# Performance work log

Measured on AMD Instinct MI355X. Metric: run time of the kernel, lower is better.

The kernel has to match this reference:

```python
import jax, jax.numpy as jnp
import numpy as np

INV_TEMPERATURE = 0.125  # 1/sqrt(head_dim=64)


def setup_inputs() -> dict:
    key = jax.random.key(0)
    kq, kk, kv, kp, km = jax.random.split(key, 5)
    B, H, S, D = 8, 8, 2048, 64
    q = jax.random.normal(kq, (B, H, S, D), dtype=jnp.float32)
    k = jax.random.normal(kk, (B, H, S, D), dtype=jnp.float32)
    v = jax.random.normal(kv, (B, H, S, D), dtype=jnp.float32)
    pos_scores = jax.random.normal(kp, (1, H, S, S), dtype=jnp.float32)
    mask = jax.random.uniform(km, (1, 1, S, S), dtype=jnp.float32)
    return {"q": q, "k": k, "v": v, "pos_scores": pos_scores, "mask": mask}


def reference(q, k, v, pos_scores, mask):
    # sim = (q k^T) * inv_temp + pos_scores, then multiplicative mask
    sim = jnp.einsum('bhid,bhjd->bhij', q, k) * INV_TEMPERATURE
    sim = mask * (sim + pos_scores)
    attn = jax.nn.softmax(sim, axis=-1)
    out = jnp.einsum('bhij,bhjd->bhid', attn, v)
    return out
```

## Files before the change

kernel.cpp:

```cpp
#include <hip/hip_runtime.h>

constexpr int SEQ = 2048;
constexpr int HD  = 64;
constexpr int NH  = 8;
constexpr int NB  = 8;
constexpr int BM  = 64;
constexpr int BN  = 64;
constexpr int KST = 72;
constexpr float INV_T = 0.125f;
constexpr float LOG2E = 1.4426950408889634f;

typedef __attribute__((ext_vector_type(8))) short bf16x8;
typedef __attribute__((ext_vector_type(8))) short s16x8;
typedef __attribute__((ext_vector_type(4))) short s16x4;
typedef __attribute__((ext_vector_type(4))) float f32x4;

__device__ __forceinline__ short f2bf(float f) {
  unsigned u = __builtin_bit_cast(unsigned, f);
  u += 0x7fffu + ((u >> 16) & 1u);
  return (short)(u >> 16);
}
__device__ __forceinline__ float bf2f(short s) {
  unsigned u = ((unsigned)(unsigned short)s) << 16;
  return __builtin_bit_cast(float, u);
}
__device__ __forceinline__ float fast_exp2(float x) {
#if __has_builtin(__builtin_amdgcn_exp2f)
  return __builtin_amdgcn_exp2f(x);
#else
  return exp2f(x);
#endif
}

__global__ __launch_bounds__(256)
void prep_kv(const float* __restrict__ k, const float* __restrict__ v,
             unsigned short* __restrict__ kb, unsigned short* __restrict__ vt)
{
  __shared__ unsigned short t[HD * KST];
  const int bh = blockIdx.y, jt = blockIdx.x, tid = threadIdx.x;
  const size_t base = (size_t)bh * SEQ * HD + (size_t)jt * BN * HD;

  {
    const float* kp = k + base + 16 * tid;
    unsigned short ko[16];
    for (int e = 0; e < 4; ++e) {
      f32x4 x = *(const f32x4*)(kp + 4 * e);
      for (int c = 0; c < 4; ++c) ko[4 * e + c] = (unsigned short)f2bf(x[c]);
    }
    *(s16x8*)(kb + base + 16 * tid)     = *(const s16x8*)&ko[0];
    *(s16x8*)(kb + base + 16 * tid + 8) = *(const s16x8*)&ko[8];
  }
  {
    const float* vp = v + base + 16 * tid;
    const int j = tid >> 2, d0 = (tid & 3) * 16;
    for (int e = 0; e < 4; ++e) {
      f32x4 x = *(const f32x4*)(vp + 4 * e);
      for (int c = 0; c < 4; ++c) t[(d0 + 4 * e + c) * KST + j] = (unsigned short)f2bf(x[c]);
    }
  }
  __syncthreads();
  {
    const int d = tid >> 2, ch = tid & 3;
    const size_t ob = (size_t)bh * HD * SEQ + (size_t)d * SEQ + jt * BN + ch * 16;
    *(s16x8*)(vt + ob)     = *(const s16x8*)&t[d * KST + ch * 16];
    *(s16x8*)(vt + ob + 8) = *(const s16x8*)&t[d * KST + ch * 16 + 8];
  }
}

__global__ __launch_bounds__(256, 4)
void attn_main(const float* __restrict__ q, const unsigned short* __restrict__ kb,
               const unsigned short* __restrict__ vt,
               const float* __restrict__ pos, const float* __restrict__ mask,
               float* __restrict__ out)
{
  __shared__ unsigned short lds_k[BN * KST];
  __shared__ unsigned short lds_v[HD * KST];

  const int n = blockIdx.x;
  const int x = n & 7, b = (n >> 3) & 7, G = n >> 6;
  const int g = G * 8 + x;
  const int h = g >> 5, it = g & 31;
  const int bh = b * NH + h;
  const int i0 = it * BM;

  const int tid = threadIdx.x, wave = tid >> 6, lane = tid & 63;
  const int quad = lane >> 4, lq = lane & 15;

  bf16x8 aq[2];
  {
    const float* qp = q + ((size_t)bh * SEQ + i0 + wave * 16 + lq) * HD + quad * 8;
    for (int k0 = 0; k0 < 2; ++k0) {
      f32x4 xv = *(const f32x4*)(qp + k0 * 32);
      f32x4 yv = *(const f32x4*)(qp + k0 * 32 + 4);
      for (int c = 0; c < 4; ++c) {
        aq[k0][c]     = f2bf(xv[c] * INV_T);
        aq[k0][4 + c] = f2bf(yv[c] * INV_T);
      }
    }
  }

  f32x4 oacc[4];
  for (int d = 0; d < 4; ++d) oacc[d] = (f32x4){0.f, 0.f, 0.f, 0.f};
  float lrun = 0.f;

  const int lw = (tid >> 3) * KST + (tid & 7) * 8;
  const unsigned short* kgb = kb + (size_t)bh * SEQ * HD + 8 * tid;
  const unsigned short* vgb = vt + (size_t)bh * HD * SEQ + (tid >> 3) * SEQ + (tid & 7) * 8;

  const int irow = i0 + wave * 16 + lq;
  const float* mrow = mask + (size_t)irow * SEQ + quad * 4;
  const float* prow = pos + ((size_t)h * SEQ + irow) * SEQ + quad * 4;

  unsigned short* lds_p = lds_k;
  const int pbase = wave * (16 * KST);

  s16x8 kx0, kx1, vx0, vx1;
  f32x4 m4[4], p4[4];

  kx0 = *(const s16x8*)(kgb);
  kx1 = *(const s16x8*)(kgb + 2048);
  vx0 = *(const s16x8*)(vgb);
  vx1 = *(const s16x8*)(vgb + 32 * SEQ);
#pragma unroll
  for (int s = 0; s < 4; ++s) {
    m4[s] = *(const f32x4*)(mrow + s * 16);
    p4[s] = *(const f32x4*)(prow + s * 16);
  }

  for (int jt = 0; jt < SEQ / BN; ++jt) {
    const int jn = (jt + 1) & 31;
    __syncthreads();
    *(s16x8*)&lds_k[lw]            = kx0;
    *(s16x8*)&lds_k[lw + 32 * KST] = kx1;
    *(s16x8*)&lds_v[lw]            = vx0;
    *(s16x8*)&lds_v[lw + 32 * KST] = vx1;
    __syncthreads();

    kx0 = *(const s16x8*)(kgb + jn * 4096);
    kx1 = *(const s16x8*)(kgb + jn * 4096 + 2048);
    vx0 = *(const s16x8*)(vgb + jn * 64);
    vx1 = *(const s16x8*)(vgb + jn * 64 + 32 * SEQ);

    f32x4 sa[4];
#pragma unroll
    for (int s = 0; s < 4; ++s) sa[s] = (f32x4){0.f, 0.f, 0.f, 0.f};
#pragma unroll
    for (int k0 = 0; k0 < 2; ++k0)
#pragma unroll
      for (int s = 0; s < 4; ++s) {
        bf16x8 bk = *(const bf16x8*)&lds_k[(s * 16 + lq) * KST + k0 * 32 + quad * 8];
        sa[s] = __builtin_amdgcn_mfma_f32_16x16x32_bf16(bk, aq[k0], sa[s], 0, 0, 0);
      }
    __syncthreads();

    const float* mjn = mrow + jn * 64;
    const float* pjn = prow + jn * 64;
#pragma unroll
    for (int s = 0; s < 4; ++s) {
      f32x4 mm = m4[s];
      f32x4 pp = p4[s];
      m4[s] = *(const f32x4*)(mjn + s * 16);
      p4[s] = *(const f32x4*)(pjn + s * 16);
      s16x4 pb;
      float ps = 0.f;
#pragma unroll
      for (int r = 0; r < 4; ++r) {
        float t = mm[r] * LOG2E;
        float a = fmaf(t, sa[s][r], t * pp[r]);
        float p = fast_exp2(a);
        unsigned pu = __builtin_bit_cast(unsigned, p);
        pb[r] = (short)(pu >> 16);
        ps += __builtin_bit_cast(float, pu & 0xffff0000u);
      }
      lrun += ps;
      *(s16x4*)&lds_p[pbase + lq * KST + s * 16 + quad * 4] = pb;
    }
    asm volatile("s_waitcnt lgkmcnt(0)" ::: "memory");

#pragma unroll
    for (int k0 = 0; k0 < 2; ++k0) {
      bf16x8 ap = *(const bf16x8*)&lds_p[pbase + lq * KST + k0 * 32 + quad * 8];
#pragma unroll
      for (int d = 0; d < 4; ++d) {
        bf16x8 bv = *(const bf16x8*)&lds_v[(d * 16 + lq) * KST + k0 * 32 + quad * 8];
        oacc[d] = __builtin_amdgcn_mfma_f32_16x16x32_bf16(ap, bv, oacc[d], 0, 0, 0);
      }
    }
  }

  lrun += __shfl_xor(lrun, 16);
  lrun += __shfl_xor(lrun, 32);

#pragma unroll
  for (int r = 0; r < 4; ++r) {
    const float lv = __shfl(lrun, quad * 4 + r);
    const float inv = 1.0f / lv;
    float* orow = out + ((size_t)bh * SEQ + i0 + wave * 16 + quad * 4 + r) * HD + lq;
#pragma unroll
    for (int d = 0; d < 4; ++d) orow[d * 16] = oacc[d][r] * inv;
  }
}

__global__ __launch_bounds__(256, 2)
void attn_fused(const float* __restrict__ q, const float* __restrict__ kk,
                const float* __restrict__ vv, const float* __restrict__ pos,
                const float* __restrict__ mask, float* __restrict__ out)
{
  __shared__ short lds_k[BN * KST];
  __shared__ short lds_v[HD * KST];
  __shared__ short lds_p[4][16 * KST];
  const int bh = blockIdx.y, h = bh & (NH - 1);
  const int i0 = blockIdx.x * BM;
  const int tid = threadIdx.x, wave = tid >> 6, lane = tid & 63;
  const int quad = lane >> 4, lq = lane & 15;
  bf16x8 aq[2];
  {
    const float* qp = q + ((size_t)bh * SEQ + i0 + wave * 16 + lq) * HD + quad * 8;
    for (int k0 = 0; k0 < 2; ++k0) {
      f32x4 xv = *(const f32x4*)(qp + k0 * 32);
      f32x4 yv = *(const f32x4*)(qp + k0 * 32 + 4);
      for (int j = 0; j < 4; ++j) { aq[k0][j] = f2bf(xv[j] * INV_T); aq[k0][4 + j] = f2bf(yv[j] * INV_T); }
    }
  }
  f32x4 oacc[4];
  for (int d = 0; d < 4; ++d) oacc[d] = (f32x4){0.f, 0.f, 0.f, 0.f};
  float mrun[4] = {-INFINITY, -INFINITY, -INFINITY, -INFINITY};
  float lrun[4] = {0.f, 0.f, 0.f, 0.f};
  const size_t kvbase = (size_t)bh * SEQ * HD;
  for (int jt = 0; jt < SEQ / BN; ++jt) {
    const int j0 = jt * BN;
    __syncthreads();
    for (int e = 0; e < 4; ++e) {
      int idx = e * 256 + tid, j = idx >> 4, d4 = (idx & 15) << 2;
      f32x4 kf = *(const f32x4*)(kk + kvbase + (size_t)(j0 + j) * HD + d4);
      s16x4 ks;
      for (int c = 0; c < 4; ++c) ks[c] = f2bf(kf[c]);
      *(s16x4*)&lds_k[j * KST + d4] = ks;
      f32x4 vf = *(const f32x4*)(vv + kvbase + (size_t)(j0 + j) * HD + d4);
      for (int c = 0; c < 4; ++c) lds_v[(d4 + c) * KST + j] = f2bf(vf[c]);
    }
    __syncthreads();
    float mk[4][4], pz[4][4];
    for (int r = 0; r < 4; ++r) {
      const int i = i0 + wave * 16 + quad * 4 + r;
      const float* mrow = mask + (size_t)i * SEQ + j0 + lq;
      const float* prow = pos + ((size_t)h * SEQ + i) * SEQ + j0 + lq;
      for (int s = 0; s < 4; ++s) { mk[r][s] = mrow[s * 16]; pz[r][s] = prow[s * 16]; }
    }
    f32x4 sa[4];
    for (int s = 0; s < 4; ++s) sa[s] = (f32x4){0.f, 0.f, 0.f, 0.f};
    for (int k0 = 0; k0 < 2; ++k0)
      for (int s = 0; s < 4; ++s) {
        bf16x8 bk = *(const bf16x8*)&lds_k[(s * 16 + lq) * KST + k0 * 32 + quad * 8];
        sa[s] = __builtin_amdgcn_mfma_f32_16x16x32_bf16(aq[k0], bk, sa[s], 0, 0, 0);
      }
    for (int r = 0; r < 4; ++r) {
      float s0 = mk[r][0] * (sa[0][r] + pz[r][0]);
      float s1 = mk[r][1] * (sa[1][r] + pz[r][1]);
      float s2 = mk[r][2] * (sa[2][r] + pz[r][2]);
      float s3 = mk[r][3] * (sa[3][r] + pz[r][3]);
      float rm = fmaxf(fmaxf(s0, s1), fmaxf(s2, s3));
      for (int off = 1; off < 16; off <<= 1) rm = fmaxf(rm, __shfl_xor(rm, off));
      float mn = fmaxf(mrun[r], rm);
      float al = __expf(mrun[r] - mn);
      mrun[r] = mn;
      short p0 = f2bf(__expf(s0 - mn)), p1 = f2bf(__expf(s1 - mn));
      short p2 = f2bf(__expf(s2 - mn)), p3 = f2bf(__expf(s3 - mn));
      float ps = bf2f(p0) + bf2f(p1) + bf2f(p2) + bf2f(p3);
      for (int off = 1; off < 16; off <<= 1) ps += __shfl_xor(ps, off);
      lrun[r] = lrun[r] * al + ps;
      for (int d = 0; d < 4; ++d) oacc[d][r] *= al;
      short* pr = &lds_p[wave][(quad * 4 + r) * KST + lq];
      pr[0] = p0; pr[16] = p1; pr[32] = p2; pr[48] = p3;
    }
    asm volatile("s_waitcnt lgkmcnt(0)" ::: "memory");
    for (int k0 = 0; k0 < 2; ++k0) {
      bf16x8 ap = *(const bf16x8*)&lds_p[wave][lq * KST + k0 * 32 + quad * 8];
      for (int d = 0; d < 4; ++d) {
        bf16x8 bv = *(const bf16x8*)&lds_v[(d * 16 + lq) * KST + k0 * 32 + quad * 8];
        oacc[d] = __builtin_amdgcn_mfma_f32_16x16x32_bf16(ap, bv, oacc[d], 0, 0, 0);
      }
    }
  }
  for (int r = 0; r < 4; ++r) {
    const int i = i0 + wave * 16 + quad * 4 + r;
    const float inv = 1.0f / lrun[r];
    float* orow = out + ((size_t)bh * SEQ + i) * HD + lq;
    for (int d = 0; d < 4; ++d) orow[d * 16] = oacc[d][r] * inv;
  }
}

extern "C" void kernel_launch(void* const* d_in, const int* in_sizes, int n_in,
                              void* d_out, int out_size, void* d_ws, size_t ws_size,
                              hipStream_t stream) {
  const float* q    = (const float*)d_in[0];
  const float* k    = (const float*)d_in[1];
  const float* v    = (const float*)d_in[2];
  const float* pos  = (const float*)d_in[3];
  const float* mask = (const float*)d_in[4];
  float* out = (float*)d_out;

  const size_t kv_elems = (size_t)NB * NH * SEQ * HD;
  const size_t kb_bytes = kv_elems * 2;
  const size_t need = 2 * kb_bytes;

  if (ws_size >= need) {
    unsigned short* kb = (unsigned short*)d_ws;
    unsigned short* vt = (unsigned short*)((char*)d_ws + kb_bytes);
    prep_kv<<<dim3(SEQ / BN, NB * NH), dim3(256), 0, stream>>>(k, v, kb, vt);
    attn_main<<<dim3(NB * NH * SEQ / BM), dim3(256), 0, stream>>>(q, kb, vt, pos, mask, out);
  } else {
    attn_fused<<<dim3(SEQ / BM, NB * NH), dim3(256), 0, stream>>>(q, k, v, pos, mask, out);
  }
}
```

Baseline: 515.7 us.

## Double-buffer K/V tiles in LDS and give P its own buffer

Allocates two LDS buffers for the K and V tiles plus a separate buffer for P. The next tile is stored into the alternate buffer while the current one is consumed, which cuts the per-iteration barriers from three to one and lets global prefetch run two tiles ahead. In exchange LDS use per block rises, which may lower occupancy below the four blocks per CU set in launch bounds, and more registers stay live.

```diff
diff --git a/kernel.cpp b/kernel.cpp
--- a/kernel.cpp
+++ b/kernel.cpp
@@ -73,8 +73,9 @@
                const float* __restrict__ pos, const float* __restrict__ mask,
                float* __restrict__ out)
 {
-  __shared__ unsigned short lds_k[BN * KST];
-  __shared__ unsigned short lds_v[HD * KST];
+  __shared__ unsigned short lds_k[2][BN * KST];
+  __shared__ unsigned short lds_v[2][HD * KST];
+  __shared__ unsigned short lds_p[4 * 16 * KST];
 
   const int n = blockIdx.x;
   const int x = n & 7, b = (n >> 3) & 7, G = n >> 6;
@@ -111,7 +112,6 @@
   const float* mrow = mask + (size_t)irow * SEQ + quad * 4;
   const float* prow = pos + ((size_t)h * SEQ + irow) * SEQ + quad * 4;
 
-  unsigned short* lds_p = lds_k;
   const int pbase = wave * (16 * KST);
 
   s16x8 kx0, kx1, vx0, vx1;
@@ -126,33 +126,41 @@
     m4[s] = *(const f32x4*)(mrow + s * 16);
     p4[s] = *(const f32x4*)(prow + s * 16);
   }
+  *(s16x8*)&lds_k[0][lw]            = kx0;
+  *(s16x8*)&lds_k[0][lw + 32 * KST] = kx1;
+  *(s16x8*)&lds_v[0][lw]            = vx0;
+  *(s16x8*)&lds_v[0][lw + 32 * KST] = vx1;
+  kx0 = *(const s16x8*)(kgb + 4096);
+  kx1 = *(const s16x8*)(kgb + 4096 + 2048);
+  vx0 = *(const s16x8*)(vgb + 64);
+  vx1 = *(const s16x8*)(vgb + 64 + 32 * SEQ);
+  __syncthreads();
 
   for (int jt = 0; jt < SEQ / BN; ++jt) {
+    const int cur = jt & 1, nxt = cur ^ 1;
+    const int j2 = (jt + 2) & 31;
+
+    f32x4 sa[4];
+#pragma unroll
+    for (int s = 0; s < 4; ++s) sa[s] = (f32x4){0.f, 0.f, 0.f, 0.f};
+#pragma unroll
+    for (int k0 = 0; k0 < 2; ++k0)
+#pragma unroll
+      for (int s = 0; s < 4; ++s) {
+        bf16x8 bk = *(const bf16x8*)&lds_k[cur][(s * 16 + lq) * KST + k0 * 32 + quad * 8];
+        sa[s] = __builtin_amdgcn_mfma_f32_16x16x32_bf16(bk, aq[k0], sa[s], 0, 0, 0);
+      }
+
+    *(s16x8*)&lds_k[nxt][lw]            = kx0;
+    *(s16x8*)&lds_k[nxt][lw + 32 * KST] = kx1;
+    *(s16x8*)&lds_v[nxt][lw]            = vx0;
+    *(s16x8*)&lds_v[nxt][lw + 32 * KST] = vx1;
+    kx0 = *(const s16x8*)(kgb + j2 * 4096);
+    kx1 = *(const s16x8*)(kgb + j2 * 4096 + 2048);
+    vx0 = *(const s16x8*)(vgb + j2 * 64);
+    vx1 = *(const s16x8*)(vgb + j2 * 64 + 32 * SEQ);
+
     const int jn = (jt + 1) & 31;
-    __syncthreads();
-    *(s16x8*)&lds_k[lw]            = kx0;
-    *(s16x8*)&lds_k[lw + 32 * KST] = kx1;
-    *(s16x8*)&lds_v[lw]            = vx0;
-    *(s16x8*)&lds_v[lw + 32 * KST] = vx1;
-    __syncthreads();
-
-    kx0 = *(const s16x8*)(kgb + jn * 4096);
-    kx1 = *(const s16x8*)(kgb + jn * 4096 + 2048);
-    vx0 = *(const s16x8*)(vgb + jn * 64);
-    vx1 = *(const s16x8*)(vgb + jn * 64 + 32 * SEQ);
-
-    f32x4 sa[4];
-#pragma unroll
-    for (int s = 0; s < 4; ++s) sa[s] = (f32x4){0.f, 0.f, 0.f, 0.f};
-#pragma unroll
-    for (int k0 = 0; k0 < 2; ++k0)
-#pragma unroll
-      for (int s = 0; s < 4; ++s) {
-        bf16x8 bk = *(const bf16x8*)&lds_k[(s * 16 + lq) * KST + k0 * 32 + quad * 8];
-        sa[s] = __builtin_amdgcn_mfma_f32_16x16x32_bf16(bk, aq[k0], sa[s], 0, 0, 0);
-      }
-    __syncthreads();
-
     const float* mjn = mrow + jn * 64;
     const float* pjn = prow + jn * 64;
 #pragma unroll
@@ -182,10 +190,12 @@
       bf16x8 ap = *(const bf16x8*)&lds_p[pbase + lq * KST + k0 * 32 + quad * 8];
 #pragma unroll
       for (int d = 0; d < 4; ++d) {
-        bf16x8 bv = *(const bf16x8*)&lds_v[(d * 16 + lq) * KST + k0 * 32 + quad * 8];
+        bf16x8 bv = *(const bf16x8*)&lds_v[cur][(d * 16 + lq) * KST + k0 * 32 + quad * 8];
         oacc[d] = __builtin_amdgcn_mfma_f32_16x16x32_bf16(ap, bv, oacc[d], 0, 0, 0);
       }
     }
+
+    __syncthreads();
   }
 
   lrun += __shfl_xor(lrun, 16);
```

Result: no change. 513.7 us (-0.4%).

## Pre-pack mask and mask*pos into bf16 pairs to halve bias traffic

Applied to the files above, without the earlier changes.

Adds a prep kernel that computes mask*log2e and mask*pos*log2e once per (h,i,j), rounds both to bf16 and packs them into one 32-bit word. The main attention kernel then streams a single dword per score instead of two fp32 loads (mask and pos), and the inner loop drops a multiply. The cost is an extra pass over the full pos tensor plus a workspace write of the packed data, and some precision lost by rounding the bias and scale to bf16. Launch bounds are also raised to target 8 waves-per-EU occupancy.

```diff
diff --git a/kernel.cpp b/kernel.cpp
--- a/kernel.cpp
+++ b/kernel.cpp
@@ -14,6 +14,7 @@
 typedef __attribute__((ext_vector_type(8))) short s16x8;
 typedef __attribute__((ext_vector_type(4))) short s16x4;
 typedef __attribute__((ext_vector_type(4))) float f32x4;
+typedef __attribute__((ext_vector_type(4))) unsigned u32x4;
 
 __device__ __forceinline__ short f2bf(float f) {
   unsigned u = __builtin_bit_cast(unsigned, f);
@@ -67,10 +68,29 @@
   }
 }
 
-__global__ __launch_bounds__(256, 4)
+__global__ __launch_bounds__(256)
+void prep_pk(const float* __restrict__ pos, const float* __restrict__ mask,
+             unsigned* __restrict__ pk)
+{
+  const size_t w = (size_t)blockIdx.x * 256 + threadIdx.x;
+  const size_t base = w * 4;
+  const size_t ij = base & (size_t)(SEQ * SEQ - 1);
+  f32x4 m = *(const f32x4*)(mask + ij);
+  f32x4 p = *(const f32x4*)(pos + base);
+  u32x4 o;
+#pragma unroll
+  for (int c = 0; c < 4; ++c) {
+    unsigned mb = (unsigned)(unsigned short)f2bf(m[c] * LOG2E);
+    unsigned pb = (unsigned)(unsigned short)f2bf(m[c] * p[c] * LOG2E);
+    o[c] = (mb << 16) | pb;
+  }
+  *(u32x4*)(pk + base) = o;
+}
+
+__global__ __launch_bounds__(256, 8)
 void attn_main(const float* __restrict__ q, const unsigned short* __restrict__ kb,
                const unsigned short* __restrict__ vt,
-               const float* __restrict__ pos, const float* __restrict__ mask,
+               const unsigned* __restrict__ pk,
                float* __restrict__ out)
 {
   __shared__ unsigned short lds_k[BN * KST];
@@ -108,24 +128,20 @@
   const unsigned short* vgb = vt + (size_t)bh * HD * SEQ + (tid >> 3) * SEQ + (tid & 7) * 8;
 
   const int irow = i0 + wave * 16 + lq;
-  const float* mrow = mask + (size_t)irow * SEQ + quad * 4;
-  const float* prow = pos + ((size_t)h * SEQ + irow) * SEQ + quad * 4;
+  const unsigned* pkrow = pk + ((size_t)h * SEQ + irow) * SEQ + quad * 4;
 
   unsigned short* lds_p = lds_k;
   const int pbase = wave * (16 * KST);
 
   s16x8 kx0, kx1, vx0, vx1;
-  f32x4 m4[4], p4[4];
+  u32x4 pk4[4];
 
   kx0 = *(const s16x8*)(kgb);
   kx1 = *(const s16x8*)(kgb + 2048);
   vx0 = *(const s16x8*)(vgb);
   vx1 = *(const s16x8*)(vgb + 32 * SEQ);
 #pragma unroll
-  for (int s = 0; s < 4; ++s) {
-    m4[s] = *(const f32x4*)(mrow + s * 16);
-    p4[s] = *(const f32x4*)(prow + s * 16);
-  }
+  for (int s = 0; s < 4; ++s) pk4[s] = *(const u32x4*)(pkrow + s * 16);
 
   for (int jt = 0; jt < SEQ / BN; ++jt) {
     const int jn = (jt + 1) & 31;
@@ -153,21 +169,19 @@
       }
     __syncthreads();
 
-    const float* mjn = mrow + jn * 64;
-    const float* pjn = prow + jn * 64;
+    const unsigned* pkn = pkrow + jn * 64;
 #pragma unroll
     for (int s = 0; s < 4; ++s) {
-      f32x4 mm = m4[s];
-      f32x4 pp = p4[s];
-      m4[s] = *(const f32x4*)(mjn + s * 16);
-      p4[s] = *(const f32x4*)(pjn + s * 16);
+      u32x4 uu = pk4[s];
+      pk4[s] = *(const u32x4*)(pkn + s * 16);
       s16x4 pb;
       float ps = 0.f;
 #pragma unroll
       for (int r = 0; r < 4; ++r) {
-        float t = mm[r] * LOG2E;
-        float a = fmaf(t, sa[s][r], t * pp[r]);
-        float p = fast_exp2(a);
+        float mf = __builtin_bit_cast(float, uu[r] & 0xffff0000u);
+        float mq = __builtin_bit_cast(float, uu[r] << 16);
+        float a  = fmaf(mf, sa[s][r], mq);
+        float p  = fast_exp2(a);
         unsigned pu = __builtin_bit_cast(unsigned, p);
         pb[r] = (short)(pu >> 16);
         ps += __builtin_bit_cast(float, pu & 0xffff0000u);
@@ -300,15 +314,18 @@
   const float* mask = (const float*)d_in[4];
   float* out = (float*)d_out;
 
-  const size_t kv_elems = (size_t)NB * NH * SEQ * HD;
-  const size_t kb_bytes = kv_elems * 2;
-  const size_t need = 2 * kb_bytes;
+  const size_t kv_elems  = (size_t)NB * NH * SEQ * HD;
+  const size_t kb_bytes  = kv_elems * 2;
+  const size_t pk_dwords = (size_t)NH * SEQ * SEQ;
+  const size_t need = 2 * kb_bytes + pk_dwords * 4;
 
   if (ws_size >= need) {
     unsigned short* kb = (unsigned short*)d_ws;
     unsigned short* vt = (unsigned short*)((char*)d_ws + kb_bytes);
+    unsigned*       pk = (unsigned*)((char*)d_ws + 2 * kb_bytes);
     prep_kv<<<dim3(SEQ / BN, NB * NH), dim3(256), 0, stream>>>(k, v, kb, vt);
-    attn_main<<<dim3(NB * NH * SEQ / BM), dim3(256), 0, stream>>>(q, kb, vt, pos, mask, out);
+    prep_pk<<<dim3((int)(pk_dwords / 4 / 256)), dim3(256), 0, stream>>>(pos, mask, pk);
+    attn_main<<<dim3(NB * NH * SEQ / BM), dim3(256), 0, stream>>>(q, kb, vt, pk, out);
   } else {
     attn_fused<<<dim3(SEQ / BM, NB * NH), dim3(256), 0, stream>>>(q, k, v, pos, mask, out);
   }
```

After: 981.1 us. 1.9x slower.
